# Kernel tuning notes

Measured on AMD Instinct MI355X. Metric: run time of the kernel, lower is better.

## Reference

```python
import math
import jax, jax.numpy as jnp
import numpy as np

B, L, H, E = 4, 2048, 16, 64
D = 64

def setup_inputs() -> dict:
    key = jax.random.key(0)
    kq, kk, kv = jax.random.split(key, 3)
    queries = jax.random.normal(kq, (B, L, H, E), dtype=jnp.float32)
    keys = jax.random.normal(kk, (B, L, H, E), dtype=jnp.float32)
    values = jax.random.normal(kv, (B, L, H, D), dtype=jnp.float32)
    return {"queries": queries, "keys": keys, "values": values}

def reference(queries, keys, values):
    # queries [B,L,H,E], keys [B,S,H,E], values [B,S,H,D]; causal => L==S
    Bq, Lq, Hq, Eq = queries.shape
    scale = 1.0 / math.sqrt(Eq)
    # scores [B,H,L,S]
    scores = jnp.einsum('blhe,bshe->bhls', queries, keys)
    S = keys.shape[1]
    causal = jnp.triu(jnp.ones((Lq, S), dtype=bool), k=1)  # True above diagonal
    scores = jnp.where(causal[None, None, :, :], -jnp.inf, scores)
    A = jax.nn.softmax(scale * scores, axis=-1)  # dropout_rate=0.0 (eval)
    V = jnp.einsum('bhls,bshd->blhd', A, values)
    return (V, A)
```

## Files before the change

### kernel.cpp

```cpp
#include <hip/hip_runtime.h>

#define B_ 4
#define L_ 2048
#define H_ 16
#define E_ 64
#define D_ 64
#define S_ 2048
#define LDP 72

typedef __bf16 bf16x8 __attribute__((ext_vector_type(8)));
typedef __bf16 bf16x4 __attribute__((ext_vector_type(4)));
typedef float  f32x4  __attribute__((ext_vector_type(4)));

__global__ __launch_bounds__(256) void fullattn_kernel(
    const float* __restrict__ Q, const float* __restrict__ K,
    const float* __restrict__ V, float* __restrict__ Vout,
    float* __restrict__ Aout)
{
    __shared__ __bf16 K_lds[64 * LDP];
    __shared__ __bf16 Vt_lds[64 * LDP];
    __shared__ __bf16 P_lds[64 * LDP];

    const int tid  = threadIdx.x;
    const int wave = tid >> 6;
    const int lane = tid & 63;
    const int ln15 = lane & 15;
    const int quad = lane >> 4;

    const int qt = blockIdx.x & 31;
    const int bh = blockIdx.x >> 5;
    const int b  = bh >> 4;
    const int h  = bh & 15;
    const int q0 = qt * 64;
    const int nb = qt + 1;

    const float SCALE = 0.125f;
    const float MSUB  = 16.0f;

    bf16x8 qfrag[2];
    {
        const int qrow = q0 + 16 * wave + ln15;
        const float* qp = Q + ((size_t)((b * L_ + qrow) * H_ + h)) * E_;
        for (int f = 0; f < 2; ++f) {
            const int e0 = quad * 8 + 32 * f;
            f32x4 x = *(const f32x4*)(qp + e0);
            f32x4 y = *(const f32x4*)(qp + e0 + 4);
            bf16x8 fr;
            fr[0] = (__bf16)x[0]; fr[1] = (__bf16)x[1];
            fr[2] = (__bf16)x[2]; fr[3] = (__bf16)x[3];
            fr[4] = (__bf16)y[0]; fr[5] = (__bf16)y[1];
            fr[6] = (__bf16)y[2]; fr[7] = (__bf16)y[3];
            qfrag[f] = fr;
        }
    }

    const float* Kbh = K + ((size_t)(b * L_) * H_ + h) * E_;
    const float* Vbh = V + ((size_t)(b * L_) * H_ + h) * D_;

    float sums[4] = {0.f, 0.f, 0.f, 0.f};
    for (int kb = 0; kb < nb; ++kb) {
        for (int i = 0; i < 4; ++i) {
            const int srow = (tid >> 4) + 16 * i;
            const float* kp = Kbh + (size_t)(kb * 64 + srow) * (H_ * E_) + (tid & 15) * 4;
            f32x4 v = *(const f32x4*)kp;
            bf16x4 bv;
            bv[0] = (__bf16)v[0]; bv[1] = (__bf16)v[1];
            bv[2] = (__bf16)v[2]; bv[3] = (__bf16)v[3];
            *(bf16x4*)&K_lds[srow * LDP + (tid & 15) * 4] = bv;
        }
        __syncthreads();
        const bool diag = (kb == qt);
        for (int t = 0; t < 4; ++t) {
            f32x4 acc = {0.f, 0.f, 0.f, 0.f};
            for (int f = 0; f < 2; ++f) {
                bf16x8 bfr = *(const bf16x8*)&K_lds[(16 * t + ln15) * LDP + quad * 8 + 32 * f];
                acc = __builtin_amdgcn_mfma_f32_16x16x32_bf16(qfrag[f], bfr, acc, 0, 0, 0);
            }
            const int scol = 16 * t + ln15;
            for (int r = 0; r < 4; ++r) {
                const int lrow = 16 * wave + quad * 4 + r;
                float p = (diag && (scol > lrow)) ? 0.0f : __expf(acc[r] * SCALE - MSUB);
                sums[r] += p;
            }
        }
        __syncthreads();
    }
    float rinv[4];
    for (int r = 0; r < 4; ++r) {
        float s = sums[r];
        s += __shfl_xor(s, 1);
        s += __shfl_xor(s, 2);
        s += __shfl_xor(s, 4);
        s += __shfl_xor(s, 8);
        rinv[r] = 1.0f / s;
    }

    f32x4 oacc[4] = {{0.f,0.f,0.f,0.f},{0.f,0.f,0.f,0.f},
                     {0.f,0.f,0.f,0.f},{0.f,0.f,0.f,0.f}};
    const size_t arow0 = (size_t)bh * L_ + q0;

    for (int kb = 0; kb < nb; ++kb) {
        for (int i = 0; i < 4; ++i) {
            const int srow = (tid >> 4) + 16 * i;
            const int c4   = (tid & 15) * 4;
            const float* kp = Kbh + (size_t)(kb * 64 + srow) * (H_ * E_) + c4;
            f32x4 kv = *(const f32x4*)kp;
            bf16x4 bv;
            bv[0] = (__bf16)kv[0]; bv[1] = (__bf16)kv[1];
            bv[2] = (__bf16)kv[2]; bv[3] = (__bf16)kv[3];
            *(bf16x4*)&K_lds[srow * LDP + c4] = bv;

            const float* vp = Vbh + (size_t)(kb * 64 + srow) * (H_ * D_) + c4;
            f32x4 vv = *(const f32x4*)vp;
            Vt_lds[(c4 + 0) * LDP + srow] = (__bf16)vv[0];
            Vt_lds[(c4 + 1) * LDP + srow] = (__bf16)vv[1];
            Vt_lds[(c4 + 2) * LDP + srow] = (__bf16)vv[2];
            Vt_lds[(c4 + 3) * LDP + srow] = (__bf16)vv[3];
        }
        __syncthreads();

        const bool diag = (kb == qt);
        for (int t = 0; t < 4; ++t) {
            f32x4 acc = {0.f, 0.f, 0.f, 0.f};
            for (int f = 0; f < 2; ++f) {
                bf16x8 bfr = *(const bf16x8*)&K_lds[(16 * t + ln15) * LDP + quad * 8 + 32 * f];
                acc = __builtin_amdgcn_mfma_f32_16x16x32_bf16(qfrag[f], bfr, acc, 0, 0, 0);
            }
            const int scol = 16 * t + ln15;
            for (int r = 0; r < 4; ++r) {
                const int lrow = 16 * wave + quad * 4 + r;
                float p = (diag && (scol > lrow)) ? 0.0f : __expf(acc[r] * SCALE - MSUB);
                P_lds[lrow * LDP + scol] = (__bf16)(p * rinv[r]);
            }
        }

        for (int i = 0; i < 4; ++i) {
            const int rl = 16 * wave + 4 * i + quad;
            bf16x4 pv = *(const bf16x4*)&P_lds[rl * LDP + ln15 * 4];
            f32x4 o;
            o[0] = (float)pv[0]; o[1] = (float)pv[1];
            o[2] = (float)pv[2]; o[3] = (float)pv[3];
            *(f32x4*)(Aout + (arow0 + rl) * S_ + kb * 64 + ln15 * 4) = o;
        }

        bf16x8 afr[2];
        for (int f = 0; f < 2; ++f)
            afr[f] = *(const bf16x8*)&P_lds[(16 * wave + ln15) * LDP + quad * 8 + 32 * f];
        for (int t = 0; t < 4; ++t)
            for (int f = 0; f < 2; ++f) {
                bf16x8 vfr = *(const bf16x8*)&Vt_lds[(16 * t + ln15) * LDP + quad * 8 + 32 * f];
                oacc[t] = __builtin_amdgcn_mfma_f32_16x16x32_bf16(afr[f], vfr, oacc[t], 0, 0, 0);
            }
        __syncthreads();
    }

    {
        const int c0 = nb * 64;
        const f32x4 z = {0.f, 0.f, 0.f, 0.f};
        for (int r = 0; r < 16; ++r) {
            float* ap = Aout + (arow0 + 16 * wave + r) * S_;
            for (int c = c0 + lane * 4; c < S_; c += 256)
                *(f32x4*)(ap + c) = z;
        }
    }

    for (int t = 0; t < 4; ++t)
        for (int r = 0; r < 4; ++r) {
            const int l = q0 + 16 * wave + quad * 4 + r;
            Vout[((size_t)(b * L_ + l) * H_ + h) * D_ + 16 * t + ln15] = oacc[t][r];
        }
}

extern "C" void kernel_launch(void* const* d_in, const int* in_sizes, int n_in,
                              void* d_out, int out_size, void* d_ws, size_t ws_size,
                              hipStream_t stream) {
    const float* Q = (const float*)d_in[0];
    const float* K = (const float*)d_in[1];
    const float* V = (const float*)d_in[2];
    float* Vout = (float*)d_out;
    float* Aout = Vout + (size_t)B_ * L_ * H_ * D_;
    dim3 grid(B_ * H_ * (L_ / 64));
    dim3 block(256);
    hipLaunchKernelGGL(fullattn_kernel, grid, block, 0, stream, Q, K, V, Vout, Aout);
}
```

Measured before the change: 1.430 ms.

## Precompute bf16 Q/K and transposed V, read MFMA fragments directly from global

Two pre-pass kernels convert Q and K to head-major bf16 and write V as a bf16 transpose into workspace. The attention kernel then loads MFMA operands straight from global memory with no LDS staging, which removes most __syncthreads and repeated fp32-to-bf16 conversion. It also reorders blocks so the largest causal tiles launch first, switches to exp2 with a fused multiply-add, and writes A directly in fp32 instead of round-tripping through bf16 in LDS. The cost is extra launches and workspace traffic, plus uncoalesced per-lane global fragment loads and scalar A stores.

```diff
diff --git a/kernel.cpp b/kernel.cpp
--- a/kernel.cpp
+++ b/kernel.cpp
@@ -12,13 +12,60 @@
 typedef __bf16 bf16x4 __attribute__((ext_vector_type(4)));
 typedef float  f32x4  __attribute__((ext_vector_type(4)));
 
+__global__ __launch_bounds__(256) void convert_qk(
+    const float* __restrict__ Q, const float* __restrict__ K,
+    __bf16* __restrict__ Qb, __bf16* __restrict__ Kb)
+{
+    const int g = blockIdx.x * 256 + threadIdx.x;
+    const float* src = blockIdx.y ? K : Q;
+    __bf16* dst = blockIdx.y ? Kb : Qb;
+    const int e4 = g & 15;
+    const int h  = (g >> 4) & (H_ - 1);
+    const int l  = (g >> 8) & (L_ - 1);
+    const int b  = g >> 19;
+    f32x4 v = *(const f32x4*)(src + (size_t)g * 4);
+    bf16x4 o;
+    o[0] = (__bf16)v[0]; o[1] = (__bf16)v[1];
+    o[2] = (__bf16)v[2]; o[3] = (__bf16)v[3];
+    *(bf16x4*)(dst + (((size_t)(b * H_ + h) * L_ + l) * E_ + e4 * 4)) = o;
+}
+
+__global__ __launch_bounds__(256) void convert_vt(
+    const float* __restrict__ V, __bf16* __restrict__ Vt)
+{
+    __shared__ __bf16 T[64 * 68];
+    const int tid = threadIdx.x;
+    const int lt  = blockIdx.x & 31;
+    const int bh  = blockIdx.x >> 5;
+    const int b = bh >> 4, h = bh & 15;
+    const int l0 = lt * 64;
+    for (int i = 0; i < 4; ++i) {
+        const int lr = (tid >> 4) + 16 * i;
+        const int c4 = (tid & 15) * 4;
+        f32x4 v = *(const f32x4*)(V + ((size_t)(b * L_ + l0 + lr) * H_ + h) * D_ + c4);
+        bf16x4 o;
+        o[0] = (__bf16)v[0]; o[1] = (__bf16)v[1];
+        o[2] = (__bf16)v[2]; o[3] = (__bf16)v[3];
+        *(bf16x4*)&T[lr * 68 + c4] = o;
+    }
+    __syncthreads();
+    for (int i = 0; i < 4; ++i) {
+        const int d  = (tid >> 4) + 16 * i;
+        const int s4 = (tid & 15) * 4;
+        bf16x4 o;
+        o[0] = T[(s4 + 0) * 68 + d];
+        o[1] = T[(s4 + 1) * 68 + d];
+        o[2] = T[(s4 + 2) * 68 + d];
+        o[3] = T[(s4 + 3) * 68 + d];
+        *(bf16x4*)(Vt + ((size_t)bh * 64 + d) * L_ + l0 + s4) = o;
+    }
+}
+
 __global__ __launch_bounds__(256) void fullattn_kernel(
-    const float* __restrict__ Q, const float* __restrict__ K,
-    const float* __restrict__ V, float* __restrict__ Vout,
+    const __bf16* __restrict__ Qb, const __bf16* __restrict__ Kb,
+    const __bf16* __restrict__ Vt, float* __restrict__ Vout,
     float* __restrict__ Aout)
 {
-    __shared__ __bf16 K_lds[64 * LDP];
-    __shared__ __bf16 Vt_lds[64 * LDP];
     __shared__ __bf16 P_lds[64 * LDP];
 
     const int tid  = threadIdx.x;
@@ -27,65 +74,49 @@
     const int ln15 = lane & 15;
     const int quad = lane >> 4;
 
-    const int qt = blockIdx.x & 31;
-    const int bh = blockIdx.x >> 5;
+    const int bh = blockIdx.x & 63;
+    const int qt = 31 - (blockIdx.x >> 6);
     const int b  = bh >> 4;
     const int h  = bh & 15;
     const int q0 = qt * 64;
     const int nb = qt + 1;
 
-    const float SCALE = 0.125f;
-    const float MSUB  = 16.0f;
+    const float C1 = 0.125f * 1.44269504089f;
+    const float C2 = -16.0f * 1.44269504089f;
+
+    const __bf16* Qh = Qb + (size_t)bh * L_ * E_;
+    const __bf16* Kh = Kb + (size_t)bh * L_ * E_;
+    const __bf16* Vh = Vt + (size_t)bh * 64 * L_;
 
     bf16x8 qfrag[2];
     {
-        const int qrow = q0 + 16 * wave + ln15;
-        const float* qp = Q + ((size_t)((b * L_ + qrow) * H_ + h)) * E_;
-        for (int f = 0; f < 2; ++f) {
-            const int e0 = quad * 8 + 32 * f;
-            f32x4 x = *(const f32x4*)(qp + e0);
-            f32x4 y = *(const f32x4*)(qp + e0 + 4);
-            bf16x8 fr;
-            fr[0] = (__bf16)x[0]; fr[1] = (__bf16)x[1];
-            fr[2] = (__bf16)x[2]; fr[3] = (__bf16)x[3];
-            fr[4] = (__bf16)y[0]; fr[5] = (__bf16)y[1];
-            fr[6] = (__bf16)y[2]; fr[7] = (__bf16)y[3];
-            qfrag[f] = fr;
-        }
-    }
-
-    const float* Kbh = K + ((size_t)(b * L_) * H_ + h) * E_;
-    const float* Vbh = V + ((size_t)(b * L_) * H_ + h) * D_;
+        const __bf16* qp = Qh + (size_t)(q0 + 16 * wave + ln15) * E_ + quad * 8;
+        qfrag[0] = *(const bf16x8*)(qp);
+        qfrag[1] = *(const bf16x8*)(qp + 32);
+    }
 
     float sums[4] = {0.f, 0.f, 0.f, 0.f};
     for (int kb = 0; kb < nb; ++kb) {
-        for (int i = 0; i < 4; ++i) {
-            const int srow = (tid >> 4) + 16 * i;
-            const float* kp = Kbh + (size_t)(kb * 64 + srow) * (H_ * E_) + (tid & 15) * 4;
-            f32x4 v = *(const f32x4*)kp;
-            bf16x4 bv;
-            bv[0] = (__bf16)v[0]; bv[1] = (__bf16)v[1];
-            bv[2] = (__bf16)v[2]; bv[3] = (__bf16)v[3];
-            *(bf16x4*)&K_lds[srow * LDP + (tid & 15) * 4] = bv;
-        }
-        __syncthreads();
         const bool diag = (kb == qt);
+        const __bf16* kp = Kh + (size_t)(kb * 64 + ln15) * E_ + quad * 8;
+#pragma unroll
         for (int t = 0; t < 4; ++t) {
+            const __bf16* kpt = kp + t * 16 * E_;
             f32x4 acc = {0.f, 0.f, 0.f, 0.f};
-            for (int f = 0; f < 2; ++f) {
-                bf16x8 bfr = *(const bf16x8*)&K_lds[(16 * t + ln15) * LDP + quad * 8 + 32 * f];
-                acc = __builtin_amdgcn_mfma_f32_16x16x32_bf16(qfrag[f], bfr, acc, 0, 0, 0);
-            }
+            acc = __builtin_amdgcn_mfma_f32_16x16x32_bf16(qfrag[0], *(const bf16x8*)(kpt), acc, 0, 0, 0);
+            acc = __builtin_amdgcn_mfma_f32_16x16x32_bf16(qfrag[1], *(const bf16x8*)(kpt + 32), acc, 0, 0, 0);
             const int scol = 16 * t + ln15;
+#pragma unroll
             for (int r = 0; r < 4; ++r) {
                 const int lrow = 16 * wave + quad * 4 + r;
-                float p = (diag && (scol > lrow)) ? 0.0f : __expf(acc[r] * SCALE - MSUB);
+                float p = (diag && (scol > lrow)) ? 0.0f
+                        : __builtin_amdgcn_exp2f(fmaf(acc[r], C1, C2));
                 sums[r] += p;
             }
         }
-        __syncthreads();
     }
     float rinv[4];
+#pragma unroll
     for (int r = 0; r < 4; ++r) {
         float s = sums[r];
         s += __shfl_xor(s, 1);
@@ -100,58 +131,35 @@
     const size_t arow0 = (size_t)bh * L_ + q0;
 
     for (int kb = 0; kb < nb; ++kb) {
-        for (int i = 0; i < 4; ++i) {
-            const int srow = (tid >> 4) + 16 * i;
-            const int c4   = (tid & 15) * 4;
-            const float* kp = Kbh + (size_t)(kb * 64 + srow) * (H_ * E_) + c4;
-            f32x4 kv = *(const f32x4*)kp;
-            bf16x4 bv;
-            bv[0] = (__bf16)kv[0]; bv[1] = (__bf16)kv[1];
-            bv[2] = (__bf16)kv[2]; bv[3] = (__bf16)kv[3];
-            *(bf16x4*)&K_lds[srow * LDP + c4] = bv;
-
-            const float* vp = Vbh + (size_t)(kb * 64 + srow) * (H_ * D_) + c4;
-            f32x4 vv = *(const f32x4*)vp;
-            Vt_lds[(c4 + 0) * LDP + srow] = (__bf16)vv[0];
-            Vt_lds[(c4 + 1) * LDP + srow] = (__bf16)vv[1];
-            Vt_lds[(c4 + 2) * LDP + srow] = (__bf16)vv[2];
-            Vt_lds[(c4 + 3) * LDP + srow] = (__bf16)vv[3];
-        }
-        __syncthreads();
-
         const bool diag = (kb == qt);
+        const __bf16* kp = Kh + (size_t)(kb * 64 + ln15) * E_ + quad * 8;
+#pragma unroll
         for (int t = 0; t < 4; ++t) {
+            const __bf16* kpt = kp + t * 16 * E_;
             f32x4 acc = {0.f, 0.f, 0.f, 0.f};
-            for (int f = 0; f < 2; ++f) {
-                bf16x8 bfr = *(const bf16x8*)&K_lds[(16 * t + ln15) * LDP + quad * 8 + 32 * f];
-                acc = __builtin_amdgcn_mfma_f32_16x16x32_bf16(qfrag[f], bfr, acc, 0, 0, 0);
-            }
+            acc = __builtin_amdgcn_mfma_f32_16x16x32_bf16(qfrag[0], *(const bf16x8*)(kpt), acc, 0, 0, 0);
+            acc = __builtin_amdgcn_mfma_f32_16x16x32_bf16(qfrag[1], *(const bf16x8*)(kpt + 32), acc, 0, 0, 0);
             const int scol = 16 * t + ln15;
+#pragma unroll
             for (int r = 0; r < 4; ++r) {
                 const int lrow = 16 * wave + quad * 4 + r;
-                float p = (diag && (scol > lrow)) ? 0.0f : __expf(acc[r] * SCALE - MSUB);
-                P_lds[lrow * LDP + scol] = (__bf16)(p * rinv[r]);
+                float p = (diag && (scol > lrow)) ? 0.0f
+                        : __builtin_amdgcn_exp2f(fmaf(acc[r], C1, C2));
+                const float a = p * rinv[r];
+                Aout[(arow0 + lrow) * S_ + kb * 64 + scol] = a;
+                P_lds[lrow * LDP + scol] = (__bf16)a;
             }
         }
 
-        for (int i = 0; i < 4; ++i) {
-            const int rl = 16 * wave + 4 * i + quad;
-            bf16x4 pv = *(const bf16x4*)&P_lds[rl * LDP + ln15 * 4];
-            f32x4 o;
-            o[0] = (float)pv[0]; o[1] = (float)pv[1];
-            o[2] = (float)pv[2]; o[3] = (float)pv[3];
-            *(f32x4*)(Aout + (arow0 + rl) * S_ + kb * 64 + ln15 * 4) = o;
-        }
-
-        bf16x8 afr[2];
-        for (int f = 0; f < 2; ++f)
-            afr[f] = *(const bf16x8*)&P_lds[(16 * wave + ln15) * LDP + quad * 8 + 32 * f];
-        for (int t = 0; t < 4; ++t)
-            for (int f = 0; f < 2; ++f) {
-                bf16x8 vfr = *(const bf16x8*)&Vt_lds[(16 * t + ln15) * LDP + quad * 8 + 32 * f];
-                oacc[t] = __builtin_amdgcn_mfma_f32_16x16x32_bf16(afr[f], vfr, oacc[t], 0, 0, 0);
-            }
-        __syncthreads();
+        bf16x8 afr0 = *(const bf16x8*)&P_lds[(16 * wave + ln15) * LDP + quad * 8];
+        bf16x8 afr1 = *(const bf16x8*)&P_lds[(16 * wave + ln15) * LDP + quad * 8 + 32];
+        const __bf16* vp = Vh + (size_t)ln15 * L_ + kb * 64 + quad * 8;
+#pragma unroll
+        for (int t = 0; t < 4; ++t) {
+            const __bf16* vpt = vp + (size_t)t * 16 * L_;
+            oacc[t] = __builtin_amdgcn_mfma_f32_16x16x32_bf16(afr0, *(const bf16x8*)(vpt), oacc[t], 0, 0, 0);
+            oacc[t] = __builtin_amdgcn_mfma_f32_16x16x32_bf16(afr1, *(const bf16x8*)(vpt + 32), oacc[t], 0, 0, 0);
+        }
     }
 
     {
@@ -164,7 +172,9 @@
         }
     }
 
+#pragma unroll
     for (int t = 0; t < 4; ++t)
+#pragma unroll
         for (int r = 0; r < 4; ++r) {
             const int l = q0 + 16 * wave + quad * 4 + r;
             Vout[((size_t)(b * L_ + l) * H_ + h) * D_ + 16 * t + ln15] = oacc[t][r];
@@ -179,7 +189,15 @@
     const float* V = (const float*)d_in[2];
     float* Vout = (float*)d_out;
     float* Aout = Vout + (size_t)B_ * L_ * H_ * D_;
-    dim3 grid(B_ * H_ * (L_ / 64));
-    dim3 block(256);
-    hipLaunchKernelGGL(fullattn_kernel, grid, block, 0, stream, Q, K, V, Vout, Aout);
-}
+
+    __bf16* Qb = (__bf16*)d_ws;
+    __bf16* Kb = Qb + (size_t)B_ * H_ * L_ * E_;
+    __bf16* Vt = Kb + (size_t)B_ * H_ * L_ * E_;
+
+    hipLaunchKernelGGL(convert_qk, dim3((B_ * L_ * H_ * E_) / (256 * 4), 2), dim3(256),
+                       0, stream, Q, K, Qb, Kb);
+    hipLaunchKernelGGL(convert_vt, dim3(B_ * H_ * (L_ / 64)), dim3(256),
+                       0, stream, V, Vt);
+    hipLaunchKernelGGL(fullattn_kernel, dim3(B_ * H_ * (L_ / 64)), dim3(256),
+                       0, stream, Qb, Kb, Vt, Vout, Aout);
+}
```

Result: slower. 1.495 ms (+4.6%).
